# Kernel optimization log

Hardware: AMD Instinct MI355X
Metric: run time of the kernel (lower is better)

Reference implementation:

```python
import jax, jax.numpy as jnp
import numpy as np

B, N, DIM, C_IN, C_OUT = 2, 512, 3, 64, 64


def setup_inputs() -> dict:
    key = jax.random.key(0)
    ks = jax.random.split(key, 9)
    geom = jax.random.normal(ks[0], (B, N, DIM, C_IN), dtype=jnp.float32)
    adj = jax.random.uniform(ks[1], (B, N, N, 1, 1), dtype=jnp.float32)
    rel = jax.random.normal(ks[2], (B, N, N, DIM, 1), dtype=jnp.float32)
    emb = jax.random.normal(ks[3], (B, N, N, 1), dtype=jnp.float32)
    # learned parameters
    theta = jax.random.normal(ks[4], (C_IN + 1, C_OUT), dtype=jnp.float32) * 0.1
    norm_w = jax.random.normal(ks[5], (C_IN + 1, 1), dtype=jnp.float32) * 0.1
    norm_b = jax.random.normal(ks[6], (1,), dtype=jnp.float32) * 0.1
    alpha = jax.random.normal(ks[7], (1, 1, C_OUT), dtype=jnp.float32) * 0.1
    beta = jax.random.normal(ks[8], (1, 1, C_OUT), dtype=jnp.float32) * 0.1
    return {
        "geometric_information": geom,
        "adjacency_matrix": adj,
        "relative_point_cloud": rel,
        "embed_pc_and_features": emb,
        "theta": theta,
        "norm_w": norm_w,
        "norm_b": norm_b,
        "alpha": alpha,
        "beta": beta,
    }


def reference(geometric_information, adjacency_matrix, relative_point_cloud,
              embed_pc_and_features, theta, norm_w, norm_b, alpha, beta):
    b, n, d, c_in = geometric_information.shape
    # broadcast sender features to all pairs: [B,n,n,3,C_in]
    g2 = jnp.broadcast_to(geometric_information[:, None], (b, n, n, d, c_in))
    # concat relative coords as an extra channel: [B,n,n,3,C_in+1]
    embed_x_and_g = jnp.concatenate([g2, relative_point_cloud], axis=-1)
    # use_all_norms branch (block_id != 0): per-channel L2 norm over spatial axis
    norms = jnp.sqrt(jnp.sum(embed_x_and_g * embed_x_and_g, axis=-2))  # [B,n,n,C_in+1]
    norm_and_feature = norms @ norm_w + norm_b + embed_pc_and_features  # [B,n,n,1]
    # P_alpha_beta: affine + activation -> [B,n,n,C_out]
    p_alpha_beta = jax.nn.relu(alpha * norm_and_feature + beta)
    # channel mixing: [B,n,n,3,C_out]
    mixed = embed_x_and_g @ theta
    # adjacency-masked sum over neighbor axis -> [B,n,3,C_out]
    out = jnp.sum(mixed * p_alpha_beta[..., None, :] * adjacency_matrix, axis=2)
    return out
```

## Files before the change

kernel.cpp:

```cpp
#include <hip/hip_runtime.h>
#include <math.h>

#define WS_S   0
#define WS_GM8 1024

typedef unsigned int u32;
typedef float f32x2 __attribute__((ext_vector_type(2)));

static __device__ __forceinline__ u32 bf16b(float x) {
    u32 u = __builtin_bit_cast(u32, x);
    return (u + 0x7FFFu + ((u >> 16) & 1u)) >> 16;
}
static __device__ __forceinline__ float blo(u32 b) {
    return __builtin_bit_cast(float, b << 16);
}
static __device__ __forceinline__ float bhi(u32 b) {
    return __builtin_bit_cast(float, b & 0xFFFF0000u);
}

__global__ __launch_bounds__(256) void prep_kernel(
    const float* __restrict__ geom,
    const float* __restrict__ theta,
    const float* __restrict__ norm_w,
    const float* __restrict__ norm_b,
    float* __restrict__ s,
    uint2* __restrict__ gm8,
    float* __restrict__ out)
{
    const int bx  = blockIdx.x;
    const int tid = threadIdx.x;

    for (int k = tid; k < 384; k += 256)
        out[(size_t)bx * 384 + k] = 0.f;

    if (bx < 256) {
        const int sub  = tid >> 6;
        const int lane = tid & 63;
        const int bj   = bx * 4 + sub;
        __shared__ float g[4][192];
        const float* gb = geom + (size_t)bj * 192;
        g[sub][lane]       = gb[lane];
        g[sub][lane + 64]  = gb[lane + 64];
        g[sub][lane + 128] = gb[lane + 128];
        __syncthreads();

        {
            float g0 = g[sub][lane], g1 = g[sub][64 + lane], g2 = g[sub][128 + lane];
            float t = sqrtf(g0 * g0 + g1 * g1 + g2 * g2) * norm_w[lane];
            for (int off = 32; off > 0; off >>= 1) t += __shfl_down(t, off);
            if (lane == 0) s[bj] = t + norm_b[0];
        }

        float a0 = 0.f, a1 = 0.f, a2 = 0.f;
        for (int c = 0; c < 64; ++c) {
            float th = theta[c * 64 + lane];
            a0 = fmaf(g[sub][c],       th, a0);
            a1 = fmaf(g[sub][64 + c],  th, a1);
            a2 = fmaf(g[sub][128 + c], th, a2);
        }
        uint2 w;
        w.x = bf16b(a0) | (bf16b(a1) << 16);
        w.y = bf16b(a2) << 16;
        gm8[(size_t)bj * 64 + lane] = w;
    }
}

__global__ __launch_bounds__(512) void main_kernel(
    const float* __restrict__ adj,
    const float* __restrict__ rel,
    const float* __restrict__ emb,
    const float* __restrict__ s_arr,
    const uint2* __restrict__ gm8,
    const float* __restrict__ theta,
    const float* __restrict__ norm_w,
    const float* __restrict__ alpha,
    const float* __restrict__ beta,
    float* __restrict__ out)
{
    const int bx   = blockIdx.x;
    const int jh   = bx & 1;
    const int iq   = (bx >> 1) & 127;
    const int b    = bx >> 8;
    const int tid  = threadIdx.x;
    const int lane = tid & 63;
    const int wv   = tid >> 6;
    const int bi0  = b * 512 + iq * 4;
    const int j0   = jh * 256;

    __shared__ uint4 pk_l[4][256];
    __shared__ float red[8][768];

    {
        const float nw64 = norm_w[64];
        #pragma unroll
        for (int u = 0; u < 2; ++u) {
            int t  = tid + u * 512;
            int il = t >> 8;
            int j  = t & 255;
            size_t p = (size_t)(bi0 + il) * 512 + j0 + j;
            const float* rp = rel + p * 3;
            float r0 = rp[0], r1 = rp[1], r2 = rp[2];
            float a   = adj[p];
            float naf = s_arr[b * 512 + j0 + j]
                      + nw64 * sqrtf(r0 * r0 + r1 * r1 + r2 * r2) + emb[p];
            uint4 q;
            q.x = __builtin_bit_cast(u32, a * naf);
            q.y = __builtin_bit_cast(u32, a);
            q.z = bf16b(r0) | (bf16b(r1) << 16);
            q.w = bf16b(r2) << 16;
            pk_l[il][j] = q;
        }
    }
    __syncthreads();

    const float al  = alpha[lane];
    const float be  = beta[lane];
    const float t64 = theta[64 * 64 + lane];
    const f32x2 t64v = {t64, t64};

    const uint2* gmv = gm8 + (size_t)(b * 512 + j0 + wv * 32) * 64 + lane;

    f32x2 acc01[4];
    float acc2[4];
    #pragma unroll
    for (int il = 0; il < 4; ++il) { acc01[il] = (f32x2){0.f, 0.f}; acc2[il] = 0.f; }

    #pragma unroll 4
    for (int jj = 0; jj < 32; ++jj) {
        uint2 gw = gmv[(size_t)jj * 64];
        const f32x2 g01 = {blo(gw.x), bhi(gw.x)};
        const float gz  = bhi(gw.y);
        #pragma unroll
        for (int il = 0; il < 4; ++il) {
            uint4 q = pk_l[il][wv * 32 + jj];
            float an = __builtin_bit_cast(float, q.x);
            float av = __builtin_bit_cast(float, q.y);
            f32x2 r01 = {blo(q.z), bhi(q.z)};
            float r2  = __builtin_bit_cast(float, q.w);
            float w  = fmaxf(fmaf(al, an, be * av), 0.f);
            f32x2 wv2 = {w, w};
            f32x2 t01 = __builtin_elementwise_fma(r01, t64v, g01);
            acc01[il] = __builtin_elementwise_fma(wv2, t01, acc01[il]);
            acc2[il]  = fmaf(w, fmaf(r2, t64, gz), acc2[il]);
        }
    }

    float* rw = &red[wv][lane];
    #pragma unroll
    for (int il = 0; il < 4; ++il) {
        rw[il * 192]       = acc01[il].x;
        rw[il * 192 + 64]  = acc01[il].y;
        rw[il * 192 + 128] = acc2[il];
    }
    __syncthreads();

    for (int k = tid; k < 768; k += 512) {
        float v = 0.f;
        #pragma unroll
        for (int w8 = 0; w8 < 8; ++w8) v += red[w8][k];
        int il = k / 192, r = k - il * 192;
        atomicAdd(&out[(size_t)(bi0 + il) * 192 + r], v);
    }
}

extern "C" void kernel_launch(void* const* d_in, const int* in_sizes, int n_in,
                              void* d_out, int out_size, void* d_ws, size_t ws_size,
                              hipStream_t stream) {
    const float* geom   = (const float*)d_in[0];
    const float* adj    = (const float*)d_in[1];
    const float* rel    = (const float*)d_in[2];
    const float* emb    = (const float*)d_in[3];
    const float* theta  = (const float*)d_in[4];
    const float* norm_w = (const float*)d_in[5];
    const float* norm_b = (const float*)d_in[6];
    const float* alpha  = (const float*)d_in[7];
    const float* beta   = (const float*)d_in[8];
    float* out = (float*)d_out;

    float* ws  = (float*)d_ws;
    float* s   = ws + WS_S;
    uint2* gm8 = (uint2*)(ws + WS_GM8);

    prep_kernel<<<512, 256, 0, stream>>>(geom, theta, norm_w, norm_b, s, gm8, out);
    main_kernel<<<512, 512, 0, stream>>>(adj, rel, emb, s, gm8, theta, norm_w,
                                         alpha, beta, out);
}
```

Measured before the change: 21.73 us.

## Give each block full neighbor range to drop output zeroing and atomics

Each main-kernel block now handles 2 receiver points across all 512 neighbors instead of 4 receivers across half the neighbors. Because the neighbor sum is no longer split between blocks, results are written directly rather than atomically added, and the prep kernel no longer zeroes the output, so it launches half the blocks. In exchange, each block loads gm8 rows for twice as many neighbors per receiver pair, so gm8 reuse per block is halved and global gm8 traffic roughly doubles.

```diff
diff --git a/kernel.cpp b/kernel.cpp
--- a/kernel.cpp
+++ b/kernel.cpp
@@ -24,45 +24,38 @@
     const float* __restrict__ norm_w,
     const float* __restrict__ norm_b,
     float* __restrict__ s,
-    uint2* __restrict__ gm8,
-    float* __restrict__ out)
+    uint2* __restrict__ gm8)
 {
-    const int bx  = blockIdx.x;
-    const int tid = threadIdx.x;
+    const int bx   = blockIdx.x;
+    const int sub  = threadIdx.x >> 6;
+    const int lane = threadIdx.x & 63;
+    const int bj   = bx * 4 + sub;
+    __shared__ float g[4][192];
 
-    for (int k = tid; k < 384; k += 256)
-        out[(size_t)bx * 384 + k] = 0.f;
+    const float* gb = geom + (size_t)bj * 192;
+    g[sub][lane]       = gb[lane];
+    g[sub][lane + 64]  = gb[lane + 64];
+    g[sub][lane + 128] = gb[lane + 128];
+    __syncthreads();
 
-    if (bx < 256) {
-        const int sub  = tid >> 6;
-        const int lane = tid & 63;
-        const int bj   = bx * 4 + sub;
-        __shared__ float g[4][192];
-        const float* gb = geom + (size_t)bj * 192;
-        g[sub][lane]       = gb[lane];
-        g[sub][lane + 64]  = gb[lane + 64];
-        g[sub][lane + 128] = gb[lane + 128];
-        __syncthreads();
+    {
+        float g0 = g[sub][lane], g1 = g[sub][64 + lane], g2 = g[sub][128 + lane];
+        float t = sqrtf(g0 * g0 + g1 * g1 + g2 * g2) * norm_w[lane];
+        for (int off = 32; off > 0; off >>= 1) t += __shfl_down(t, off);
+        if (lane == 0) s[bj] = t + norm_b[0];
+    }
 
-        {
-            float g0 = g[sub][lane], g1 = g[sub][64 + lane], g2 = g[sub][128 + lane];
-            float t = sqrtf(g0 * g0 + g1 * g1 + g2 * g2) * norm_w[lane];
-            for (int off = 32; off > 0; off >>= 1) t += __shfl_down(t, off);
-            if (lane == 0) s[bj] = t + norm_b[0];
-        }
-
-        float a0 = 0.f, a1 = 0.f, a2 = 0.f;
-        for (int c = 0; c < 64; ++c) {
-            float th = theta[c * 64 + lane];
-            a0 = fmaf(g[sub][c],       th, a0);
-            a1 = fmaf(g[sub][64 + c],  th, a1);
-            a2 = fmaf(g[sub][128 + c], th, a2);
-        }
-        uint2 w;
-        w.x = bf16b(a0) | (bf16b(a1) << 16);
-        w.y = bf16b(a2) << 16;
-        gm8[(size_t)bj * 64 + lane] = w;
+    float a0 = 0.f, a1 = 0.f, a2 = 0.f;
+    for (int c = 0; c < 64; ++c) {
+        float th = theta[c * 64 + lane];
+        a0 = fmaf(g[sub][c],       th, a0);
+        a1 = fmaf(g[sub][64 + c],  th, a1);
+        a2 = fmaf(g[sub][128 + c], th, a2);
     }
+    uint2 w;
+    w.x = bf16b(a0) | (bf16b(a1) << 16);
+    w.y = bf16b(a2) << 16;
+    gm8[(size_t)bj * 64 + lane] = w;
 }
 
 __global__ __launch_bounds__(512) void main_kernel(
@@ -78,30 +71,28 @@
     float* __restrict__ out)
 {
     const int bx   = blockIdx.x;
-    const int jh   = bx & 1;
-    const int iq   = (bx >> 1) & 127;
+    const int ip   = bx & 255;
     const int b    = bx >> 8;
     const int tid  = threadIdx.x;
     const int lane = tid & 63;
     const int wv   = tid >> 6;
-    const int bi0  = b * 512 + iq * 4;
-    const int j0   = jh * 256;
+    const int bi0  = b * 512 + ip * 2;
 
-    __shared__ uint4 pk_l[4][256];
-    __shared__ float red[8][768];
+    __shared__ uint4 pk_l[2][512];
+    __shared__ float red[8][384];
 
     {
         const float nw64 = norm_w[64];
         #pragma unroll
         for (int u = 0; u < 2; ++u) {
             int t  = tid + u * 512;
-            int il = t >> 8;
-            int j  = t & 255;
-            size_t p = (size_t)(bi0 + il) * 512 + j0 + j;
+            int il = t >> 9;
+            int j  = t & 511;
+            size_t p = (size_t)(bi0 + il) * 512 + j;
             const float* rp = rel + p * 3;
             float r0 = rp[0], r1 = rp[1], r2 = rp[2];
             float a   = adj[p];
-            float naf = s_arr[b * 512 + j0 + j]
+            float naf = s_arr[b * 512 + j]
                       + nw64 * sqrtf(r0 * r0 + r1 * r1 + r2 * r2) + emb[p];
             uint4 q;
             q.x = __builtin_bit_cast(u32, a * naf);
@@ -118,21 +109,21 @@
     const float t64 = theta[64 * 64 + lane];
     const f32x2 t64v = {t64, t64};
 
-    const uint2* gmv = gm8 + (size_t)(b * 512 + j0 + wv * 32) * 64 + lane;
+    const uint2* gmv = gm8 + (size_t)(b * 512 + wv * 64) * 64 + lane;
 
-    f32x2 acc01[4];
-    float acc2[4];
+    f32x2 acc01[2];
+    float acc2[2];
     #pragma unroll
-    for (int il = 0; il < 4; ++il) { acc01[il] = (f32x2){0.f, 0.f}; acc2[il] = 0.f; }
+    for (int il = 0; il < 2; ++il) { acc01[il] = (f32x2){0.f, 0.f}; acc2[il] = 0.f; }
 
     #pragma unroll 4
-    for (int jj = 0; jj < 32; ++jj) {
+    for (int jj = 0; jj < 64; ++jj) {
         uint2 gw = gmv[(size_t)jj * 64];
         const f32x2 g01 = {blo(gw.x), bhi(gw.x)};
         const float gz  = bhi(gw.y);
         #pragma unroll
-        for (int il = 0; il < 4; ++il) {
-            uint4 q = pk_l[il][wv * 32 + jj];
+        for (int il = 0; il < 2; ++il) {
+            uint4 q = pk_l[il][wv * 64 + jj];
             float an = __builtin_bit_cast(float, q.x);
             float av = __builtin_bit_cast(float, q.y);
             f32x2 r01 = {blo(q.z), bhi(q.z)};
@@ -147,19 +138,19 @@
 
     float* rw = &red[wv][lane];
     #pragma unroll
-    for (int il = 0; il < 4; ++il) {
+    for (int il = 0; il < 2; ++il) {
         rw[il * 192]       = acc01[il].x;
         rw[il * 192 + 64]  = acc01[il].y;
         rw[il * 192 + 128] = acc2[il];
     }
     __syncthreads();
 
-    for (int k = tid; k < 768; k += 512) {
+    if (tid < 384) {
         float v = 0.f;
         #pragma unroll
-        for (int w8 = 0; w8 < 8; ++w8) v += red[w8][k];
-        int il = k / 192, r = k - il * 192;
-        atomicAdd(&out[(size_t)(bi0 + il) * 192 + r], v);
+        for (int w8 = 0; w8 < 8; ++w8) v += red[w8][tid];
+        int il = tid / 192, r = tid - il * 192;
+        out[(size_t)(bi0 + il) * 192 + r] = v;
     }
 }
 
@@ -181,7 +172,7 @@
     float* s   = ws + WS_S;
     uint2* gm8 = (uint2*)(ws + WS_GM8);
 
-    prep_kernel<<<512, 256, 0, stream>>>(geom, theta, norm_w, norm_b, s, gm8, out);
+    prep_kernel<<<256, 256, 0, stream>>>(geom, theta, norm_w, norm_b, s, gm8);
     main_kernel<<<512, 512, 0, stream>>>(adj, rel, emb, s, gm8, theta, norm_w,
                                          alpha, beta, out);
 }
```

Result: slower. 23.38 us (+7.6%).
